# Kernel optimization log

Measured on AMD Instinct MI355X. Metric: run time of the kernel, lower is better.

The kernel has to match this reference:

```python
import jax, jax.numpy as jnp
import numpy as np

PARAMETER = 0.1
INPUT_SIZE = 512
OUTPUT_SIZE = 512


def setup_inputs() -> dict:
    key = jax.random.key(0)
    k1, k2, k3 = jax.random.split(key, 3)
    T, B = 4096, 32
    input_tensor = jax.random.normal(k1, (T, B, INPUT_SIZE), dtype=jnp.float32)
    k = np.sqrt(1.0 / INPUT_SIZE)
    weight = jax.random.uniform(k2, (OUTPUT_SIZE, INPUT_SIZE), dtype=jnp.float32, minval=-k, maxval=k)
    bias = jax.random.uniform(k3, (OUTPUT_SIZE,), dtype=jnp.float32, minval=-k, maxval=k)
    return {"input_tensor": input_tensor, "weight": weight, "bias": bias}


def reference(input_tensor, weight, bias):
    # linear projection: [T, B, I] @ [I, O] -> [T, B, O]
    y = jnp.einsum('tbi,oi->tbo', input_tensor, weight) + bias

    # EMA recurrence: v[0] = y[0]; v[t] = p * v[t-1] + y[t]
    def step(carry, yt):
        v = PARAMETER * carry + yt
        return v, v

    _, rest = jax.lax.scan(step, y[0], y[1:])
    return jnp.concatenate([y[:1], rest], axis=0)
```

## Files before the change

### kernel.cpp

```cpp
#include <hip/hip_runtime.h>
#include <hip/hip_bf16.h>

#define T_DIM 4096
#define B_DIM 32
#define I_DIM 512
#define O_DIM 512
#define M_DIM (T_DIM * B_DIM)
#define PARAM 0.1f
#define ISCALE 1.1111112f

#define STRIP 64
#define TAPS 8

#define BM 64
#define BN 256
#define BK 64

typedef __attribute__((ext_vector_type(8))) short bf16x8;
typedef __attribute__((ext_vector_type(4))) float f32x4;

__device__ __forceinline__ unsigned short f2bf(float f) {
    union { __hip_bfloat16 b; unsigned short u; } cv;
    cv.b = __float2bfloat16(f);
    return cv.u;
}

__global__ __launch_bounds__(256) void wcvt_kernel(const float* __restrict__ W,
                                                   unsigned short* __restrict__ Wb) {
    const int i = (blockIdx.x * 256 + threadIdx.x) * 4;
    f32x4 v = *(const f32x4*)(W + i);
    ushort4 o;
    o.x = f2bf(v[0]); o.y = f2bf(v[1]); o.z = f2bf(v[2]); o.w = f2bf(v[3]);
    *(ushort4*)(Wb + i) = o;
}

__global__ __launch_bounds__(256) void xema_kernel(const float* __restrict__ X,
                                                   unsigned short* __restrict__ Xv) {
    const int s   = blockIdx.x >> 4;
    const int blk = blockIdx.x & 15;
    const int col = (blk * 256 + threadIdx.x) * 4;
    const int t0  = s * STRIP;
    const int b   = col >> 9;
    const int o   = col & 511;

    const float* xin = X + (size_t)t0 * 16384 + col;
    unsigned short* xout = Xv + (size_t)(t0 * 32 + b) * 512 + o;

    f32x4 v = {0.f, 0.f, 0.f, 0.f};
    if (s > 0) {
        const float* w = xin - (size_t)TAPS * 16384;
        #pragma unroll
        for (int j = 0; j < TAPS; ++j)
            v = PARAM * v + *(const f32x4*)(w + (size_t)j * 16384);
    }

    f32x4 bufA[8], bufB[8];
    #pragma unroll
    for (int j = 0; j < 8; ++j) bufA[j] = *(const f32x4*)(xin + (size_t)j * 16384);

    #pragma unroll
    for (int i = 0; i < STRIP; i += 16) {
        #pragma unroll
        for (int j = 0; j < 8; ++j)
            bufB[j] = *(const f32x4*)(xin + (size_t)(i + 8 + j) * 16384);
        #pragma unroll
        for (int j = 0; j < 8; ++j) {
            v = PARAM * v + bufA[j];
            ushort4 pk; pk.x = f2bf(v[0]); pk.y = f2bf(v[1]); pk.z = f2bf(v[2]); pk.w = f2bf(v[3]);
            *(ushort4*)(xout + (size_t)(i + j) * 16384) = pk;
        }
        if (i + 16 < STRIP) {
            #pragma unroll
            for (int j = 0; j < 8; ++j)
                bufA[j] = *(const f32x4*)(xin + (size_t)(i + 16 + j) * 16384);
        }
        #pragma unroll
        for (int j = 0; j < 8; ++j) {
            v = PARAM * v + bufB[j];
            ushort4 pk; pk.x = f2bf(v[0]); pk.y = f2bf(v[1]); pk.z = f2bf(v[2]); pk.w = f2bf(v[3]);
            *(ushort4*)(xout + (size_t)(i + 8 + j) * 16384) = pk;
        }
    }
}

__global__ __launch_bounds__(512, 4) void gemm_kernel(const unsigned short* __restrict__ Xv,
                                                      const unsigned short* __restrict__ Wb,
                                                      const float* __restrict__ bias,
                                                      float* __restrict__ Y) {
    __shared__ __align__(16) short As[2][BM * BK];
    __shared__ __align__(16) short Bs[2][BN * BK];

    const int tid  = threadIdx.x;
    const int lane = tid & 63;
    const int wave = tid >> 6;

    const int bid = blockIdx.x;
    const int jj  = bid >> 3;
    const int bn  = jj & 1;
    const int mt  = (bid & 7) * 256 + (jj >> 1);
    const int row0 = mt * BM;
    const int col0 = bn * BN;

    const int cs = (tid & 7) ^ ((tid >> 3) & 7);
    const unsigned short* aSrc = Xv + (size_t)(row0 + (tid >> 3)) * 512 + cs * 8;
    const unsigned short* bSrc = Wb + (size_t)(col0 + (tid >> 3)) * 512 + cs * 8;

    #define STAGE(buf, k0)                                                          \
        do {                                                                        \
            __builtin_amdgcn_global_load_lds(                                       \
                (const __attribute__((address_space(1))) unsigned int*)(aSrc + (k0)),\
                (__attribute__((address_space(3))) unsigned int*)(&As[buf][0] + wave * 512), \
                16, 0, 0);                                                          \
            _Pragma("unroll")                                                       \
            for (int i_ = 0; i_ < 4; ++i_) {                                        \
                __builtin_amdgcn_global_load_lds(                                   \
                    (const __attribute__((address_space(1))) unsigned int*)(bSrc + (size_t)i_ * 64 * 512 + (k0)), \
                    (__attribute__((address_space(3))) unsigned int*)(&Bs[buf][0] + i_ * 4096 + wave * 512), \
                    16, 0, 0);                                                      \
            }                                                                       \
        } while (0)

    f32x4 acc[4][2] = {};

    STAGE(0, 0);
    __syncthreads();

    #pragma unroll
    for (int ks = 0; ks < I_DIM / BK; ++ks) {
        const int cur = ks & 1;
        if (ks < I_DIM / BK - 1)
            STAGE(cur ^ 1, (ks + 1) * BK);

        #pragma unroll
        for (int kk = 0; kk < 2; ++kk) {
            const int cc = kk * 4 + (lane >> 4);
            bf16x8 a[4], b[2];
            #pragma unroll
            for (int mf = 0; mf < 4; ++mf) {
                const int r = mf * 16 + (lane & 15);
                a[mf] = *(const bf16x8*)((const char*)&As[cur][0] + r * 128 + ((cc ^ (r & 7)) << 4));
            }
            #pragma unroll
            for (int nf = 0; nf < 2; ++nf) {
                const int r = wave * 32 + nf * 16 + (lane & 15);
                b[nf] = *(const bf16x8*)((const char*)&Bs[cur][0] + r * 128 + ((cc ^ (r & 7)) << 4));
            }
            #pragma unroll
            for (int mf = 0; mf < 4; ++mf)
                #pragma unroll
                for (int nf = 0; nf < 2; ++nf)
                    acc[mf][nf] = __builtin_amdgcn_mfma_f32_16x16x32_bf16(
                        a[mf], b[nf], acc[mf][nf], 0, 0, 0);
        }
        __syncthreads();
    }

    float sc[4][4];
    #pragma unroll
    for (int mf = 0; mf < 4; ++mf)
        #pragma unroll
        for (int j = 0; j < 4; ++j) {
            const int t = (row0 + mf * 16 + ((lane >> 4) << 2) + j) >> 5;
            sc[mf][j] = (1.0f - __expf(-2.3025851f * (float)(t + 1))) * ISCALE;
        }

    #pragma unroll
    for (int mf = 0; mf < 4; ++mf) {
        #pragma unroll
        for (int nf = 0; nf < 2; ++nf) {
            const int gcol = col0 + wave * 32 + nf * 16 + (lane & 15);
            const float bv = bias[gcol];
            #pragma unroll
            for (int j = 0; j < 4; ++j) {
                const int grow = row0 + mf * 16 + ((lane >> 4) << 2) + j;
                Y[(size_t)grow * O_DIM + gcol] = acc[mf][nf][j] + sc[mf][j] * bv;
            }
        }
    }
}

extern "C" void kernel_launch(void* const* d_in, const int* in_sizes, int n_in,
                              void* d_out, int out_size, void* d_ws, size_t ws_size,
                              hipStream_t stream) {
    const float* X    = (const float*)d_in[0];
    const float* W    = (const float*)d_in[1];
    const float* bias = (const float*)d_in[2];
    float* Y = (float*)d_out;
    unsigned short* Wb = (unsigned short*)d_ws;
    unsigned short* Xv = (unsigned short*)((char*)d_ws + (1 << 20));

    wcvt_kernel<<<dim3(O_DIM * I_DIM / (256 * 4)), dim3(256), 0, stream>>>(W, Wb);
    xema_kernel<<<dim3((T_DIM / STRIP) * 16), dim3(256), 0, stream>>>(X, Xv);
    gemm_kernel<<<dim3((M_DIM / BM) * (O_DIM / BN)), dim3(512), 0, stream>>>(Xv, Wb, bias, Y);
}
```

Measured before the change: 260.8 us.

## Enlarge GEMM tile to 128x256 with triple-buffered LDS pipeline

The GEMM tile grows from 64x256 to 128x256, and the eight waves are arranged 2x4, each computing a 64x64 sub-tile with 16 accumulators. This raises operand reuse per LDS load. The k-loop is unrolled by hand and uses three LDS buffers, prefetching three stages ahead. Explicit vmcnt waits and raw s_barrier calls replace __syncthreads, and s_setprio is raised around the MFMA blocks. In exchange it uses more LDS and registers, so occupancy drops from 4 to 2 blocks per CU, and the hand-coded vmcnt counts must match the number of issued loads.

```diff
diff --git a/kernel.cpp b/kernel.cpp
--- a/kernel.cpp
+++ b/kernel.cpp
@@ -12,9 +12,10 @@
 #define STRIP 64
 #define TAPS 8
 
-#define BM 64
+#define BM 128
 #define BN 256
 #define BK 64
+#define NK (I_DIM / BK)
 
 typedef __attribute__((ext_vector_type(8))) short bf16x8;
 typedef __attribute__((ext_vector_type(4))) float f32x4;
@@ -83,21 +84,23 @@
     }
 }
 
-__global__ __launch_bounds__(512, 4) void gemm_kernel(const unsigned short* __restrict__ Xv,
+__global__ __launch_bounds__(512, 2) void gemm_kernel(const unsigned short* __restrict__ Xv,
                                                       const unsigned short* __restrict__ Wb,
                                                       const float* __restrict__ bias,
                                                       float* __restrict__ Y) {
-    __shared__ __align__(16) short As[2][BM * BK];
-    __shared__ __align__(16) short Bs[2][BN * BK];
+    __shared__ __align__(16) short As[3][BM * BK];
+    __shared__ __align__(16) short Bs[3][BN * BK];
 
     const int tid  = threadIdx.x;
     const int lane = tid & 63;
     const int wave = tid >> 6;
+    const int wm   = wave >> 2;
+    const int wn   = wave & 3;
 
     const int bid = blockIdx.x;
-    const int jj  = bid >> 3;
-    const int bn  = jj & 1;
-    const int mt  = (bid & 7) * 256 + (jj >> 1);
+    const int j   = bid >> 3;
+    const int bn  = j & 1;
+    const int mt  = (bid & 7) * 128 + (j >> 1);
     const int row0 = mt * BM;
     const int col0 = bn * BN;
 
@@ -105,75 +108,96 @@
     const unsigned short* aSrc = Xv + (size_t)(row0 + (tid >> 3)) * 512 + cs * 8;
     const unsigned short* bSrc = Wb + (size_t)(col0 + (tid >> 3)) * 512 + cs * 8;
 
-    #define STAGE(buf, k0)                                                          \
-        do {                                                                        \
-            __builtin_amdgcn_global_load_lds(                                       \
-                (const __attribute__((address_space(1))) unsigned int*)(aSrc + (k0)),\
-                (__attribute__((address_space(3))) unsigned int*)(&As[buf][0] + wave * 512), \
-                16, 0, 0);                                                          \
-            _Pragma("unroll")                                                       \
-            for (int i_ = 0; i_ < 4; ++i_) {                                        \
-                __builtin_amdgcn_global_load_lds(                                   \
-                    (const __attribute__((address_space(1))) unsigned int*)(bSrc + (size_t)i_ * 64 * 512 + (k0)), \
-                    (__attribute__((address_space(3))) unsigned int*)(&Bs[buf][0] + i_ * 4096 + wave * 512), \
-                    16, 0, 0);                                                      \
-            }                                                                       \
+    #define STAGE(buf, k0)                                                            \
+        do {                                                                          \
+            _Pragma("unroll")                                                         \
+            for (int it_ = 0; it_ < 2; ++it_)                                         \
+                __builtin_amdgcn_global_load_lds(                                     \
+                    (const __attribute__((address_space(1))) unsigned int*)(aSrc + (size_t)it_ * 64 * 512 + (k0)), \
+                    (__attribute__((address_space(3))) unsigned int*)(&As[buf][0] + (it_ * 512 + wave * 64) * 8),  \
+                    16, 0, 0);                                                        \
+            _Pragma("unroll")                                                         \
+            for (int it_ = 0; it_ < 4; ++it_)                                         \
+                __builtin_amdgcn_global_load_lds(                                     \
+                    (const __attribute__((address_space(1))) unsigned int*)(bSrc + (size_t)it_ * 64 * 512 + (k0)), \
+                    (__attribute__((address_space(3))) unsigned int*)(&Bs[buf][0] + (it_ * 512 + wave * 64) * 8),  \
+                    16, 0, 0);                                                        \
         } while (0)
 
-    f32x4 acc[4][2] = {};
-
-    STAGE(0, 0);
-    __syncthreads();
-
-    #pragma unroll
-    for (int ks = 0; ks < I_DIM / BK; ++ks) {
-        const int cur = ks & 1;
-        if (ks < I_DIM / BK - 1)
-            STAGE(cur ^ 1, (ks + 1) * BK);
-
-        #pragma unroll
-        for (int kk = 0; kk < 2; ++kk) {
-            const int cc = kk * 4 + (lane >> 4);
-            bf16x8 a[4], b[2];
-            #pragma unroll
-            for (int mf = 0; mf < 4; ++mf) {
-                const int r = mf * 16 + (lane & 15);
-                a[mf] = *(const bf16x8*)((const char*)&As[cur][0] + r * 128 + ((cc ^ (r & 7)) << 4));
-            }
-            #pragma unroll
-            for (int nf = 0; nf < 2; ++nf) {
-                const int r = wave * 32 + nf * 16 + (lane & 15);
-                b[nf] = *(const bf16x8*)((const char*)&Bs[cur][0] + r * 128 + ((cc ^ (r & 7)) << 4));
-            }
-            #pragma unroll
-            for (int mf = 0; mf < 4; ++mf)
-                #pragma unroll
-                for (int nf = 0; nf < 2; ++nf)
-                    acc[mf][nf] = __builtin_amdgcn_mfma_f32_16x16x32_bf16(
-                        a[mf], b[nf], acc[mf][nf], 0, 0, 0);
-        }
-        __syncthreads();
-    }
+    f32x4 acc[4][4] = {};
+
+    #define COMPUTE(buf)                                                              \
+        do {                                                                          \
+            _Pragma("unroll")                                                         \
+            for (int kk = 0; kk < 2; ++kk) {                                          \
+                const int cc = kk * 4 + (lane >> 4);                                  \
+                bf16x8 a_[4], b_[4];                                                  \
+                _Pragma("unroll")                                                     \
+                for (int mf = 0; mf < 4; ++mf) {                                      \
+                    const int r = wm * 64 + mf * 16 + (lane & 15);                    \
+                    a_[mf] = *(const bf16x8*)((const char*)&As[buf][0] + r * 128 + ((cc ^ (r & 7)) << 4)); \
+                }                                                                     \
+                _Pragma("unroll")                                                     \
+                for (int nf = 0; nf < 4; ++nf) {                                      \
+                    const int r = wn * 64 + nf * 16 + (lane & 15);                    \
+                    b_[nf] = *(const bf16x8*)((const char*)&Bs[buf][0] + r * 128 + ((cc ^ (r & 7)) << 4)); \
+                }                                                                     \
+                __builtin_amdgcn_s_setprio(1);                                        \
+                _Pragma("unroll")                                                     \
+                for (int mf = 0; mf < 4; ++mf)                                        \
+                    _Pragma("unroll")                                                 \
+                    for (int nf = 0; nf < 4; ++nf)                                    \
+                        acc[mf][nf] = __builtin_amdgcn_mfma_f32_16x16x32_bf16(        \
+                            a_[mf], b_[nf], acc[mf][nf], 0, 0, 0);                    \
+                __builtin_amdgcn_s_setprio(0);                                        \
+            }                                                                         \
+        } while (0)
+
+    #define KITER(k, vm, buf)                                                         \
+        do {                                                                          \
+            asm volatile("s_waitcnt vmcnt(" #vm ")" ::: "memory");                    \
+            __builtin_amdgcn_sched_barrier(0);                                        \
+            __builtin_amdgcn_s_barrier();                                             \
+            asm volatile("" ::: "memory");                                            \
+            COMPUTE(buf);                                                             \
+            asm volatile("" ::: "memory");                                            \
+            __builtin_amdgcn_s_barrier();                                             \
+            asm volatile("" ::: "memory");                                            \
+            if ((k) + 3 < NK) STAGE(buf, ((k) + 3) * BK);                             \
+        } while (0)
+
+    STAGE(0, 0 * BK);
+    STAGE(1, 1 * BK);
+    STAGE(2, 2 * BK);
+
+    KITER(0, 12, 0);
+    KITER(1, 12, 1);
+    KITER(2, 12, 2);
+    KITER(3, 12, 0);
+    KITER(4, 12, 1);
+    KITER(5, 12, 2);
+    KITER(6,  6, 0);
+    KITER(7,  0, 1);
 
     float sc[4][4];
     #pragma unroll
     for (int mf = 0; mf < 4; ++mf)
         #pragma unroll
-        for (int j = 0; j < 4; ++j) {
-            const int t = (row0 + mf * 16 + ((lane >> 4) << 2) + j) >> 5;
-            sc[mf][j] = (1.0f - __expf(-2.3025851f * (float)(t + 1))) * ISCALE;
+        for (int jj = 0; jj < 4; ++jj) {
+            const int t = (row0 + wm * 64 + mf * 16 + ((lane >> 4) << 2) + jj) >> 5;
+            sc[mf][jj] = (1.0f - __expf(-2.3025851f * (float)(t + 1))) * ISCALE;
         }
 
     #pragma unroll
     for (int mf = 0; mf < 4; ++mf) {
         #pragma unroll
-        for (int nf = 0; nf < 2; ++nf) {
-            const int gcol = col0 + wave * 32 + nf * 16 + (lane & 15);
+        for (int nf = 0; nf < 4; ++nf) {
+            const int gcol = col0 + wn * 64 + nf * 16 + (lane & 15);
             const float bv = bias[gcol];
             #pragma unroll
-            for (int j = 0; j < 4; ++j) {
-                const int grow = row0 + mf * 16 + ((lane >> 4) << 2) + j;
-                Y[(size_t)grow * O_DIM + gcol] = acc[mf][nf][j] + sc[mf][j] * bv;
+            for (int jj = 0; jj < 4; ++jj) {
+                const int grow = row0 + wm * 64 + mf * 16 + ((lane >> 4) << 2) + jj;
+                Y[(size_t)grow * O_DIM + gcol] = acc[mf][nf][jj] + sc[mf][jj] * bv;
             }
         }
     }
```

New measurement: 240.5 us. 7.8% less time.
